# Kernel tuning notes

Hardware: AMD Instinct MI355X
Metric: run time of the kernel (lower is better)

Reference implementation:

```python
import jax, jax.numpy as jnp
import numpy as np

B, S, D = 2, 2048, 1024
H = 16
HD = D // H  # 64
ROPE_BASE = 10000.0


def rotate_half(x):
    x1, x2 = jnp.split(x, 2, axis=-1)
    return jnp.concatenate((-x2, x1), axis=-1)


def rope_cos_sin(seq_len, dim, dtype):
    inv_freq = 1.0 / (ROPE_BASE ** (jnp.arange(0, dim, 2, dtype=jnp.float32) / dim))
    t = jnp.arange(seq_len, dtype=jnp.float32)
    freqs = jnp.einsum('i,j->ij', t, inv_freq)          # [S, dim/2]
    emb = jnp.concatenate((freqs, freqs), axis=-1)      # [S, dim]
    return jnp.cos(emb).astype(dtype), jnp.sin(emb).astype(dtype)


def setup_inputs() -> dict:
    key = jax.random.key(0)
    ks = jax.random.split(key, 5)
    std = 0.02
    return {
        'x': jax.random.normal(ks[0], (B, S, D), dtype=jnp.float32),
        'wq': jax.random.normal(ks[1], (D, D), dtype=jnp.float32) * std,
        'wk': jax.random.normal(ks[2], (D, D), dtype=jnp.float32) * std,
        'wv': jax.random.normal(ks[3], (D, D), dtype=jnp.float32) * std,
        'wo': jax.random.normal(ks[4], (D, D), dtype=jnp.float32) * std,
    }


def reference(x, wq, wk, wv, wo):
    b, s, d = x.shape
    # Q/K/V projections (nn.Linear: x @ W.T)
    q = jnp.einsum('bsd,ed->bse', x, wq).reshape(b, s, H, HD).transpose(0, 2, 1, 3)
    k = jnp.einsum('bsd,ed->bse', x, wk).reshape(b, s, H, HD).transpose(0, 2, 1, 3)
    v = jnp.einsum('bsd,ed->bse', x, wv).reshape(b, s, H, HD).transpose(0, 2, 1, 3)
    # RoPE
    cos, sin = rope_cos_sin(s, HD, x.dtype)  # [s, HD]
    cos = cos[None, None]  # [1,1,s,HD]
    sin = sin[None, None]
    q = q * cos + rotate_half(q) * sin
    k = k * cos + rotate_half(k) * sin
    # Causal SDPA
    scale = HD ** -0.5
    scores = jnp.einsum('bhqd,bhkd->bhqk', q, k) * scale
    causal = jnp.tril(jnp.ones((s, s), dtype=bool))
    scores = jnp.where(causal[None, None], scores, jnp.finfo(scores.dtype).min)
    attn = jax.nn.softmax(scores, axis=-1)
    out = jnp.einsum('bhqk,bhkd->bhqd', attn, v)
    out = out.transpose(0, 2, 1, 3).reshape(b, s, d)
    return jnp.einsum('bsd,ed->bse', out, wo)
```

## Files before the change

kernel.cpp:

```cpp
#include <hip/hip_runtime.h>
#include <hip/hip_bf16.h>
#include <cstdint>
#include <cstddef>

#define BDIM 2
#define SDIM 2048
#define DDIM 1024
#define HN   16
#define HDIM 64

using bf16 = __bf16;
typedef __attribute__((ext_vector_type(8))) __bf16 bf16x8;
typedef __attribute__((ext_vector_type(4))) __bf16 bf16x4;
typedef __attribute__((ext_vector_type(8))) unsigned short ushort8;
typedef __attribute__((ext_vector_type(4))) float  f32x4;

#define MFMA16(a, b, c) __builtin_amdgcn_mfma_f32_16x16x32_bf16((a), (b), (c), 0, 0, 0)

#define ASYNC16(g, l)                                                          \
  __builtin_amdgcn_global_load_lds(                                            \
      (const __attribute__((address_space(1))) void*)(g),                      \
      (__attribute__((address_space(3))) void*)(l), 16, 0, 0)

#define QSCALE 0.1803368801111204f

__global__ __launch_bounds__(256) void cvt_bf16(const float* __restrict__ src,
                                                bf16* __restrict__ dst, int n4) {
  int i = blockIdx.x * 256 + threadIdx.x;
  if (i < n4) {
    float4 v = ((const float4*)src)[i];
    bf16x4 o = {(__bf16)v.x, (__bf16)v.y, (__bf16)v.z, (__bf16)v.w};
    *(bf16x4*)(dst + (size_t)i * 4) = o;
  }
}

struct Ptr4 { const float* p[4]; };
__global__ __launch_bounds__(256) void cvt_w(Ptr4 srcs, bf16* __restrict__ dst) {
  const int seg = blockIdx.y;
  const float* src = srcs.p[seg];
  int i = blockIdx.x * 256 + threadIdx.x;
  float4 v = ((const float4*)src)[i];
  bf16x4 o = {(__bf16)v.x, (__bf16)v.y, (__bf16)v.z, (__bf16)v.w};
  *(bf16x4*)(dst + (size_t)seg * (DDIM * DDIM) + (size_t)i * 4) = o;
}

__global__ __launch_bounds__(256) void rope_table(float* __restrict__ cosT,
                                                  float* __restrict__ sinT) {
  int i = blockIdx.x * 256 + threadIdx.x;
  int s = i >> 5, j = i & 31;
  float inv = powf(10000.f, -(float)j * (1.f / 32.f));
  float a = (float)s * inv;
  float sn, c;
  sincosf(a, &sn, &c);
  cosT[s * 64 + j]      = c;
  cosT[s * 64 + j + 32] = c;
  sinT[s * 64 + j]      = sn;
  sinT[s * 64 + j + 32] = sn;
}

__global__ __launch_bounds__(256) void rope_apply(bf16* __restrict__ q,
                                                  bf16* __restrict__ k,
                                                  const float* __restrict__ cosT,
                                                  const float* __restrict__ sinT) {
  int i = blockIdx.x * 256 + threadIdx.x;
  int j = i & 31;
  int s = (i >> 5) & (SDIM - 1);
  int bh = i >> 16;
  size_t base = ((size_t)bh * SDIM + s) * HDIM;
  float c = cosT[s * 64 + j], sn = sinT[s * 64 + j];
  float a = (float)q[base + j], b2 = (float)q[base + j + 32];
  q[base + j]      = (__bf16)((a * c - b2 * sn) * QSCALE);
  q[base + j + 32] = (__bf16)((b2 * c + a * sn) * QSCALE);
  a = (float)k[base + j]; b2 = (float)k[base + j + 32];
  k[base + j]      = (__bf16)(a * c - b2 * sn);
  k[base + j + 32] = (__bf16)(b2 * c + a * sn);
}

__global__ __launch_bounds__(256) void transpose_v(const unsigned short* __restrict__ v,
                                                   unsigned short* __restrict__ vt) {
  const int bh = blockIdx.y;
  const int s_base = blockIdx.x * 32 + (threadIdx.x >> 6) * 8;
  const int d = threadIdx.x & 63;
  const unsigned short* src = v + ((size_t)bh * SDIM + s_base) * HDIM + d;
  ushort8 o;
#pragma unroll
  for (int j = 0; j < 8; ++j) o[j] = src[(size_t)j * HDIM];
  *(ushort8*)(vt + ((size_t)bh * HDIM + d) * SDIM + s_base) = o;
}

template <int MODE>
__global__ __launch_bounds__(256) void gemm_bt(const bf16* __restrict__ A,
                                               const bf16* __restrict__ B0,
                                               void* __restrict__ C0) {
  constexpr int K = 1024;
  __shared__ __align__(16) bf16 As[128 * 64];
  __shared__ __align__(16) bf16 Bs[128 * 64];
  const int tid = threadIdx.x;
  const int l = tid & 63, w = tid >> 6;
  const int wr = w >> 1, wc = w & 1;
  const int lr = l & 15, lg = l >> 4;
  const int bm = blockIdx.y * 128;
  const int bn = blockIdx.x * 128;
  const bf16* Bw = B0 + (size_t)blockIdx.z * (1024 * 1024);

  f32x4 acc[4][4] = {};

  for (int k0 = 0; k0 < K; k0 += 64) {
    __syncthreads();
#pragma unroll
    for (int i = 0; i < 4; ++i) {
      int idx = i * 2048 + tid * 8;
      int row = idx >> 6, col = idx & 63;
      ASYNC16(A + (size_t)(bm + row) * K + (k0 + col), As + idx);
      ASYNC16(Bw + (size_t)(bn + row) * K + (k0 + col), Bs + idx);
    }
    __syncthreads();
#pragma unroll
    for (int c = 0; c < 2; ++c) {
      bf16x8 af[4], bfr[4];
#pragma unroll
      for (int m = 0; m < 4; ++m)
        af[m] = *(const bf16x8*)(As + (wr * 64 + m * 16 + lr) * 64 + c * 32 + lg * 8);
#pragma unroll
      for (int n = 0; n < 4; ++n)
        bfr[n] = *(const bf16x8*)(Bs + (wc * 64 + n * 16 + lr) * 64 + c * 32 + lg * 8);
      __builtin_amdgcn_s_setprio(1);
#pragma unroll
      for (int m = 0; m < 4; ++m)
#pragma unroll
        for (int n = 0; n < 4; ++n)
          acc[m][n] = MFMA16(af[m], bfr[n], acc[m][n]);
      __builtin_amdgcn_s_setprio(0);
    }
  }

#pragma unroll
  for (int m = 0; m < 4; ++m) {
#pragma unroll
    for (int n = 0; n < 4; ++n) {
#pragma unroll
      for (int r = 0; r < 4; ++r) {
        int row = bm + wr * 64 + m * 16 + lg * 4 + r;
        int col = bn + wc * 64 + n * 16 + lr;
        float v = acc[m][n][r];
        if constexpr (MODE == 0) {
          bf16* C = (bf16*)C0 + (size_t)blockIdx.z * ((size_t)BDIM * SDIM * DDIM);
          size_t off = (((size_t)(row >> 11) * HN + (col >> 6)) * SDIM + (row & (SDIM - 1))) * HDIM + (col & 63);
          C[off] = (__bf16)v;
        } else {
          ((float*)C0)[(size_t)row * DDIM + col] = v;
        }
      }
    }
  }
}

__global__ __launch_bounds__(256) void attn_fwd(const bf16* __restrict__ qg,
                                                const bf16* __restrict__ kg,
                                                const bf16* __restrict__ vtg,
                                                bf16* __restrict__ og) {
  __shared__ __align__(16) bf16 Ks[2][8 * 512];
  __shared__ __align__(16) bf16 Vs[2][8 * 512];
  __shared__ __align__(16) bf16 Pl[4][16 * 64];

  const int tid = threadIdx.x;
  const int l = tid & 63, w = tid >> 6;
  const int lr = l & 15, lg = l >> 4;
  const int bh = blockIdx.x;
  const int qt = 31 - blockIdx.y;
  const int q0 = qt * 64;
  const size_t hb = (size_t)bh * SDIM * HDIM;
  const bf16* Q  = qg + hb;
  const bf16* Kp = kg + hb;
  const bf16* Vp = vtg + hb;
  const int b = bh >> 4, h = bh & 15;
  bf16* Pw = &Pl[w][0];
  const int swz = lr & 7;

  const int mm0 = 2 * w, mm1 = 2 * w + 1;
  const int f0 = mm0 & 3, c0 = mm0 >> 2;
  const int f1 = mm1 & 3, c1 = mm1 >> 2;

  bf16x8 qf[2];
#pragma unroll
  for (int c = 0; c < 2; ++c)
    qf[c] = *(const bf16x8*)(Q + (size_t)(q0 + w * 16 + lr) * HDIM + c * 32 + lg * 8);

  f32x4 o[4] = {};
  float m = -3e38f, lsum = 0.f;

  const bf16* kN0 = Kp + (size_t)(f0 * 16 + lr) * HDIM + c0 * 32 + lg * 8;
  const bf16* kN1 = Kp + (size_t)(f1 * 16 + lr) * HDIM + c1 * 32 + lg * 8;
  const bf16* vN0 = Vp + (size_t)(f0 * 16 + lr) * SDIM + c0 * 32 + lg * 8;
  const bf16* vN1 = Vp + (size_t)(f1 * 16 + lr) * SDIM + c1 * 32 + lg * 8;

  ASYNC16(kN0, Ks[0] + mm0 * 512 + l * 8); kN0 += 64 * HDIM;
  ASYNC16(kN1, Ks[0] + mm1 * 512 + l * 8); kN1 += 64 * HDIM;
  ASYNC16(vN0, Vs[0] + mm0 * 512 + l * 8); vN0 += 64;
  ASYNC16(vN1, Vs[0] + mm1 * 512 + l * 8); vN1 += 64;
  __syncthreads();

  for (int t = 0; t <= qt; ++t) {
    const int cur = t & 1;
    if (t < qt) {
      bf16* kd = Ks[cur ^ 1];
      bf16* vd = Vs[cur ^ 1];
      ASYNC16(kN0, kd + mm0 * 512 + l * 8); kN0 += 64 * HDIM;
      ASYNC16(kN1, kd + mm1 * 512 + l * 8); kN1 += 64 * HDIM;
      ASYNC16(vN0, vd + mm0 * 512 + l * 8); vN0 += 64;
      ASYNC16(vN1, vd + mm1 * 512 + l * 8); vN1 += 64;
    }

    const bool diag = (t == qt);
    const int fLim = diag ? w : 3;

    f32x4 sc[4] = {};
    __builtin_amdgcn_s_setprio(1);
#pragma unroll
    for (int c = 0; c < 2; ++c)
#pragma unroll
      for (int f = 0; f < 4; ++f)
        if (f <= fLim) {
          bf16x8 kfr = *(const bf16x8*)(Ks[cur] + (c * 4 + f) * 512 + l * 8);
          sc[f] = MFMA16(kfr, qf[c], sc[f]);
        }
    __builtin_amdgcn_s_setprio(0);

    if (diag) {
#pragma unroll
      for (int f = 0; f < 4; ++f)
#pragma unroll
        for (int r = 0; r < 4; ++r) {
          if (f > w)
            sc[f][r] = -3e38f;
          else if (f == w)
            sc[f][r] = (lg * 4 + r <= lr) ? sc[f][r] : -3e38f;
        }
    }

    float mxl = -3e38f;
#pragma unroll
    for (int f = 0; f < 4; ++f)
#pragma unroll
      for (int r = 0; r < 4; ++r) mxl = fmaxf(mxl, sc[f][r]);

    if (!__all(mxl - m <= 8.f)) {
      float mx = fmaxf(mxl, __shfl_xor(mxl, 16));
      mx = fmaxf(mx, __shfl_xor(mx, 32));
      float mnew = fmaxf(m, mx);
      float corr = exp2f(m - mnew);
      m = mnew;
      lsum *= corr;
      float cb[4];
#pragma unroll
      for (int r = 0; r < 4; ++r) cb[r] = __shfl(corr, lg * 4 + r);
#pragma unroll
      for (int n = 0; n < 4; ++n)
#pragma unroll
        for (int r = 0; r < 4; ++r) o[n][r] *= cb[r];
    }

    float rs = 0.f;
#pragma unroll
    for (int f = 0; f < 4; ++f) {
      float p0 = exp2f(sc[f][0] - m);
      float p1 = exp2f(sc[f][1] - m);
      float p2 = exp2f(sc[f][2] - m);
      float p3 = exp2f(sc[f][3] - m);
      rs += (p0 + p1) + (p2 + p3);
      bf16x4 pv = {(__bf16)p0, (__bf16)p1, (__bf16)p2, (__bf16)p3};
      const int ch = f * 2 + (lg >> 1);
      *(bf16x4*)(Pw + lr * 64 + ((ch ^ swz) << 3) + (lg & 1) * 4) = pv;
    }
    rs += __shfl_xor(rs, 16);
    rs += __shfl_xor(rs, 32);
    lsum += rs;

    const int cLim = diag ? (w >> 1) : 1;
    __builtin_amdgcn_s_setprio(1);
#pragma unroll
    for (int c = 0; c < 2; ++c)
      if (c <= cLim) {
        bf16x8 pf = *(const bf16x8*)(Pw + lr * 64 + (((c * 4 + lg) ^ swz) << 3));
#pragma unroll
        for (int n = 0; n < 4; ++n) {
          bf16x8 vfr = *(const bf16x8*)(Vs[cur] + (c * 4 + n) * 512 + l * 8);
          o[n] = MFMA16(pf, vfr, o[n]);
        }
      }
    __builtin_amdgcn_s_setprio(0);

    __syncthreads();
  }

  float lb[4];
#pragma unroll
  for (int r = 0; r < 4; ++r) lb[r] = __shfl(lsum, lg * 4 + r);
#pragma unroll
  for (int r = 0; r < 4; ++r) {
    float rl = 1.f / lb[r];
    int qr = q0 + 16 * w + lg * 4 + r;
#pragma unroll
    for (int n = 0; n < 4; ++n)
      og[((size_t)(b * SDIM + qr)) * DDIM + h * HDIM + n * 16 + lr] =
          (__bf16)(o[n][r] * rl);
  }
}

extern "C" void kernel_launch(void* const* d_in, const int* in_sizes, int n_in,
                              void* d_out, int out_size, void* d_ws, size_t ws_size,
                              hipStream_t stream) {
  const float* x  = (const float*)d_in[0];
  const float* wq = (const float*)d_in[1];
  const float* wk = (const float*)d_in[2];
  const float* wv = (const float*)d_in[3];
  const float* wo = (const float*)d_in[4];

  char* ws = (char*)d_ws;
  const size_t MB = 1024 * 1024;
  bf16* xb   = (bf16*)(ws + 0);
  bf16* wqb  = (bf16*)(ws + 8 * MB);
  bf16* wob  = (bf16*)(ws + 14 * MB);
  bf16* qb   = (bf16*)(ws + 16 * MB);
  bf16* kb   = (bf16*)(ws + 24 * MB);
  bf16* vb   = (bf16*)(ws + 32 * MB);
  bf16* ob   = (bf16*)(ws + 40 * MB);
  float* cosT = (float*)(ws + 48 * MB);
  float* sinT = (float*)(ws + 49 * MB);
  bf16* vtb  = xb;

  const int NX = BDIM * SDIM * DDIM;
  const int NW = DDIM * DDIM;

  cvt_bf16<<<NX / 4 / 256, 256, 0, stream>>>(x, xb, NX / 4);
  Ptr4 wsrc{{wq, wk, wv, wo}};
  cvt_w<<<dim3(NW / 4 / 256, 4), 256, 0, stream>>>(wsrc, wqb);
  rope_table<<<(SDIM * 32) / 256, 256, 0, stream>>>(cosT, sinT);
  gemm_bt<0><<<dim3(8, 32, 3), 256, 0, stream>>>(xb, wqb, (void*)qb);
  rope_apply<<<(32 * SDIM * 32) / 256, 256, 0, stream>>>(qb, kb, cosT, sinT);
  transpose_v<<<dim3(SDIM / 32, 32), 256, 0, stream>>>((const unsigned short*)vb,
                                                       (unsigned short*)vtb);
  attn_fwd<<<dim3(32, 32), 256, 0, stream>>>(qb, kb, vtb, ob);
  gemm_bt<1><<<dim3(8, 32, 1), 256, 0, stream>>>(ob, wob, d_out);
}
```

Measured before the change: 145.8 us.

## Fuse RoPE and V transpose kernels; rotate three LDS buffers in attention

Merges the RoPE application and V transpose into one vectorized kernel, so one launch replaces two and q/k are read and written as 4-wide bf16 vectors instead of scalars. In the attention kernel, K and V double buffers (4 tiles) become a 3-slot rotating buffer, which cuts LDS use. The next V tile is now loaded into the slot just freed by K after an extra mid-iteration barrier. This may allow higher occupancy, at the cost of an additional __syncthreads per tile and a shorter lead time for V prefetch.

```diff
diff --git a/kernel.cpp b/kernel.cpp
--- a/kernel.cpp
+++ b/kernel.cpp
@@ -58,34 +58,54 @@
   sinT[s * 64 + j + 32] = sn;
 }
 
-__global__ __launch_bounds__(256) void rope_apply(bf16* __restrict__ q,
-                                                  bf16* __restrict__ k,
-                                                  const float* __restrict__ cosT,
-                                                  const float* __restrict__ sinT) {
-  int i = blockIdx.x * 256 + threadIdx.x;
-  int j = i & 31;
-  int s = (i >> 5) & (SDIM - 1);
-  int bh = i >> 16;
-  size_t base = ((size_t)bh * SDIM + s) * HDIM;
-  float c = cosT[s * 64 + j], sn = sinT[s * 64 + j];
-  float a = (float)q[base + j], b2 = (float)q[base + j + 32];
-  q[base + j]      = (__bf16)((a * c - b2 * sn) * QSCALE);
-  q[base + j + 32] = (__bf16)((b2 * c + a * sn) * QSCALE);
-  a = (float)k[base + j]; b2 = (float)k[base + j + 32];
-  k[base + j]      = (__bf16)(a * c - b2 * sn);
-  k[base + j + 32] = (__bf16)(b2 * c + a * sn);
-}
-
-__global__ __launch_bounds__(256) void transpose_v(const unsigned short* __restrict__ v,
-                                                   unsigned short* __restrict__ vt) {
+__global__ __launch_bounds__(256) void fixup_qkv(bf16* __restrict__ q,
+                                                 bf16* __restrict__ k,
+                                                 const unsigned short* __restrict__ v,
+                                                 unsigned short* __restrict__ vt,
+                                                 const float* __restrict__ cosT,
+                                                 const float* __restrict__ sinT) {
   const int bh = blockIdx.y;
-  const int s_base = blockIdx.x * 32 + (threadIdx.x >> 6) * 8;
-  const int d = threadIdx.x & 63;
-  const unsigned short* src = v + ((size_t)bh * SDIM + s_base) * HDIM + d;
-  ushort8 o;
-#pragma unroll
-  for (int j = 0; j < 8; ++j) o[j] = src[(size_t)j * HDIM];
-  *(ushort8*)(vt + ((size_t)bh * HDIM + d) * SDIM + s_base) = o;
+  const int s0 = blockIdx.x * 32;
+  const int tid = threadIdx.x;
+
+  {
+    const int s = s0 + (tid >> 3);
+    const int j0 = (tid & 7) * 4;
+    const size_t base = ((size_t)bh * SDIM + s) * HDIM;
+    const float4 c4 = *(const float4*)(cosT + s * 64 + j0);
+    const float4 s4 = *(const float4*)(sinT + s * 64 + j0);
+    const float cc[4] = {c4.x, c4.y, c4.z, c4.w};
+    const float ss[4] = {s4.x, s4.y, s4.z, s4.w};
+
+    bf16x4 qlo = *(bf16x4*)(q + base + j0);
+    bf16x4 qhi = *(bf16x4*)(q + base + j0 + 32);
+    bf16x4 klo = *(bf16x4*)(k + base + j0);
+    bf16x4 khi = *(bf16x4*)(k + base + j0 + 32);
+    bf16x4 rql, rqh, rkl, rkh;
+#pragma unroll
+    for (int e = 0; e < 4; ++e) {
+      float a = (float)qlo[e], b = (float)qhi[e];
+      rql[e] = (__bf16)((a * cc[e] - b * ss[e]) * QSCALE);
+      rqh[e] = (__bf16)((b * cc[e] + a * ss[e]) * QSCALE);
+      a = (float)klo[e]; b = (float)khi[e];
+      rkl[e] = (__bf16)(a * cc[e] - b * ss[e]);
+      rkh[e] = (__bf16)(b * cc[e] + a * ss[e]);
+    }
+    *(bf16x4*)(q + base + j0)      = rql;
+    *(bf16x4*)(q + base + j0 + 32) = rqh;
+    *(bf16x4*)(k + base + j0)      = rkl;
+    *(bf16x4*)(k + base + j0 + 32) = rkh;
+  }
+
+  {
+    const int w = tid >> 6, d = tid & 63;
+    const int sb = s0 + w * 8;
+    const unsigned short* src = v + ((size_t)bh * SDIM + sb) * HDIM + d;
+    ushort8 o;
+#pragma unroll
+    for (int j = 0; j < 8; ++j) o[j] = src[(size_t)j * HDIM];
+    *(ushort8*)(vt + ((size_t)bh * HDIM + d) * SDIM + sb) = o;
+  }
 }
 
 template <int MODE>
@@ -159,9 +179,8 @@
                                                 const bf16* __restrict__ kg,
                                                 const bf16* __restrict__ vtg,
                                                 bf16* __restrict__ og) {
-  __shared__ __align__(16) bf16 Ks[2][8 * 512];
-  __shared__ __align__(16) bf16 Vs[2][8 * 512];
-  __shared__ __align__(16) bf16 Pl[4][16 * 64];
+  __shared__ __align__(16) bf16 Sl[3][4096];
+  __shared__ __align__(16) bf16 Pl[4][1024];
 
   const int tid = threadIdx.x;
   const int l = tid & 63, w = tid >> 6;
@@ -180,6 +199,8 @@
   const int mm0 = 2 * w, mm1 = 2 * w + 1;
   const int f0 = mm0 & 3, c0 = mm0 >> 2;
   const int f1 = mm1 & 3, c1 = mm1 >> 2;
+  const int lo0 = mm0 * 512 + l * 8;
+  const int lo1 = mm1 * 512 + l * 8;
 
   bf16x8 qf[2];
 #pragma unroll
@@ -194,21 +215,18 @@
   const bf16* vN0 = Vp + (size_t)(f0 * 16 + lr) * SDIM + c0 * 32 + lg * 8;
   const bf16* vN1 = Vp + (size_t)(f1 * 16 + lr) * SDIM + c1 * 32 + lg * 8;
 
-  ASYNC16(kN0, Ks[0] + mm0 * 512 + l * 8); kN0 += 64 * HDIM;
-  ASYNC16(kN1, Ks[0] + mm1 * 512 + l * 8); kN1 += 64 * HDIM;
-  ASYNC16(vN0, Vs[0] + mm0 * 512 + l * 8); vN0 += 64;
-  ASYNC16(vN1, Vs[0] + mm1 * 512 + l * 8); vN1 += 64;
+  ASYNC16(kN0, Sl[0] + lo0); kN0 += 64 * HDIM;
+  ASYNC16(kN1, Sl[0] + lo1); kN1 += 64 * HDIM;
+  ASYNC16(vN0, Sl[1] + lo0); vN0 += 64;
+  ASYNC16(vN1, Sl[1] + lo1); vN1 += 64;
   __syncthreads();
 
+  int ks = 0, vs = 1;
   for (int t = 0; t <= qt; ++t) {
-    const int cur = t & 1;
+    const int kn = 3 - ks - vs;
     if (t < qt) {
-      bf16* kd = Ks[cur ^ 1];
-      bf16* vd = Vs[cur ^ 1];
-      ASYNC16(kN0, kd + mm0 * 512 + l * 8); kN0 += 64 * HDIM;
-      ASYNC16(kN1, kd + mm1 * 512 + l * 8); kN1 += 64 * HDIM;
-      ASYNC16(vN0, vd + mm0 * 512 + l * 8); vN0 += 64;
-      ASYNC16(vN1, vd + mm1 * 512 + l * 8); vN1 += 64;
+      ASYNC16(kN0, Sl[kn] + lo0); kN0 += 64 * HDIM;
+      ASYNC16(kN1, Sl[kn] + lo1); kN1 += 64 * HDIM;
     }
 
     const bool diag = (t == qt);
@@ -221,10 +239,16 @@
 #pragma unroll
       for (int f = 0; f < 4; ++f)
         if (f <= fLim) {
-          bf16x8 kfr = *(const bf16x8*)(Ks[cur] + (c * 4 + f) * 512 + l * 8);
+          bf16x8 kfr = *(const bf16x8*)(Sl[ks] + (c * 4 + f) * 512 + l * 8);
           sc[f] = MFMA16(kfr, qf[c], sc[f]);
         }
     __builtin_amdgcn_s_setprio(0);
+
+    __syncthreads();
+    if (t < qt) {
+      ASYNC16(vN0, Sl[ks] + lo0); vN0 += 64;
+      ASYNC16(vN1, Sl[ks] + lo1); vN1 += 64;
+    }
 
     if (diag) {
 #pragma unroll
@@ -284,13 +308,15 @@
         bf16x8 pf = *(const bf16x8*)(Pw + lr * 64 + (((c * 4 + lg) ^ swz) << 3));
 #pragma unroll
         for (int n = 0; n < 4; ++n) {
-          bf16x8 vfr = *(const bf16x8*)(Vs[cur] + (c * 4 + n) * 512 + l * 8);
+          bf16x8 vfr = *(const bf16x8*)(Sl[vs] + (c * 4 + n) * 512 + l * 8);
           o[n] = MFMA16(pf, vfr, o[n]);
         }
       }
     __builtin_amdgcn_s_setprio(0);
 
     __syncthreads();
+    vs = ks;
+    ks = kn;
   }
 
   float lb[4];
@@ -337,9 +363,8 @@
   cvt_w<<<dim3(NW / 4 / 256, 4), 256, 0, stream>>>(wsrc, wqb);
   rope_table<<<(SDIM * 32) / 256, 256, 0, stream>>>(cosT, sinT);
   gemm_bt<0><<<dim3(8, 32, 3), 256, 0, stream>>>(xb, wqb, (void*)qb);
-  rope_apply<<<(32 * SDIM * 32) / 256, 256, 0, stream>>>(qb, kb, cosT, sinT);
-  transpose_v<<<dim3(SDIM / 32, 32), 256, 0, stream>>>((const unsigned short*)vb,
-                                                       (unsigned short*)vtb);
+  fixup_qkv<<<dim3(SDIM / 32, 32), 256, 0, stream>>>(qb, kb, (const unsigned short*)vb,
+                                                     (unsigned short*)vtb, cosT, sinT);
   attn_fwd<<<dim3(32, 32), 256, 0, stream>>>(qb, kb, vtb, ob);
   gemm_bt<1><<<dim3(8, 32, 1), 256, 0, stream>>>(ob, wob, d_out);
 }
```

Result: faster. 142.5 us (-2.3%).
